# Performance work log

Measured on AMD Instinct MI355X. Metric: run time of the kernel, lower is better.

Reference implementation:

```python
import jax, jax.numpy as jnp
import numpy as np

N = 50000
E = 800000
IN_C = 1024
HID = 64
HEADS = 4
OUT_C = 64
NEG_SLOPE = 0.2  # PyG GATConv default


def setup_inputs() -> dict:
    key = jax.random.key(0)
    ks = jax.random.split(key, 12)
    x = jax.random.normal(ks[0], (N, IN_C), dtype=jnp.float32)
    edge_index = jax.random.randint(ks[1], (2, E), 0, N, dtype=jnp.int64)
    s1 = 1.0 / np.sqrt(IN_C)
    s2 = 1.0 / np.sqrt(HEADS * HID)
    return {
        "x": x,
        "edge_index": edge_index,
        "W1": jax.random.normal(ks[2], (HEADS * HID, IN_C), dtype=jnp.float32) * s1,
        "a_src1": jax.random.normal(ks[3], (HEADS, HID), dtype=jnp.float32) * s2,
        "a_dst1": jax.random.normal(ks[4], (HEADS, HID), dtype=jnp.float32) * s2,
        "b1": jnp.zeros((HEADS * HID,), dtype=jnp.float32),
        "W2": jax.random.normal(ks[5], (OUT_C, HEADS * HID), dtype=jnp.float32) * s2,
        "a_src2": jax.random.normal(ks[6], (1, OUT_C), dtype=jnp.float32) * 0.1,
        "a_dst2": jax.random.normal(ks[7], (1, OUT_C), dtype=jnp.float32) * 0.1,
        "b2": jnp.zeros((OUT_C,), dtype=jnp.float32),
    }


def gat_conv(x, src, dst, W, a_src, a_dst, b, heads, concat):
    # x: [N, F_in]; src/dst: [E'] (self-loops already appended)
    n = x.shape[0]
    h = (x @ W.T).reshape(n, heads, -1)                 # [N, H, C]
    alpha_s = (h * a_src).sum(-1)                       # [N, H]
    alpha_d = (h * a_dst).sum(-1)                       # [N, H]
    e = jax.nn.leaky_relu(alpha_s[src] + alpha_d[dst], NEG_SLOPE)  # [E', H]
    # segment softmax over edges grouped by destination
    m = jax.ops.segment_max(e, dst, num_segments=n)     # [N, H]
    ex = jnp.exp(e - m[dst])
    denom = jax.ops.segment_sum(ex, dst, num_segments=n)
    alpha = ex / denom[dst]                             # [E', H]
    out = jax.ops.segment_sum(alpha[:, :, None] * h[src], dst, num_segments=n)  # [N, H, C]
    out = out.reshape(n, -1) if concat else out.mean(axis=1)
    return out + b


def reference(x, edge_index, W1, a_src1, a_dst1, b1, W2, a_src2, a_dst2, b2):
    n = x.shape[0]
    loop = jnp.arange(n, dtype=edge_index.dtype)
    src = jnp.concatenate([edge_index[0], loop])  # PyG add_self_loops=True
    dst = jnp.concatenate([edge_index[1], loop])
    # eval mode: dropout is identity
    h = gat_conv(x, src, dst, W1, a_src1, a_dst1, b1, HEADS, concat=True)
    h = jax.nn.elu(h)
    out = gat_conv(h, src, dst, W2, a_src2, a_dst2, b2, 1, concat=False)
    return out
```

## Files before the change

### kernel.cpp

```cpp
#include <hip/hip_runtime.h>
#include <hip/hip_bf16.h>
#include <math.h>

constexpr int IN_C = 1024;
constexpr int HEADS = 4;
constexpr int F1 = 256;
constexpr int OUT_C = 64;
constexpr float NEG = 0.2f;

using bf16x8 = __attribute__((ext_vector_type(8))) short;
using f32x4 = __attribute__((ext_vector_type(4))) float;

__device__ __forceinline__ float leaky(float x) { return x > 0.f ? x : NEG * x; }

__device__ __forceinline__ unsigned short bf16bits(float v) {
  __hip_bfloat16 b = __float2bfloat16(v);
  return *reinterpret_cast<unsigned short*>(&b);
}
__device__ __forceinline__ float bf2f(unsigned short u) {
  union { unsigned u; float f; } c; c.u = (unsigned)u << 16; return c.f;
}

#define GLD_LDS16(g, l)                                                        \
  __builtin_amdgcn_global_load_lds(                                            \
      (const __attribute__((address_space(1))) void*)(g),                      \
      (__attribute__((address_space(3))) void*)(l), 16, 0, 0)

__global__ void cvt_bf16_kernel(const float* __restrict__ in,
                                unsigned short* __restrict__ out, int n) {
  int i = blockIdx.x * blockDim.x + threadIdx.x;
  if (i < n) out[i] = bf16bits(in[i]);
}

constexpr int LDTA = 72;

__global__ __launch_bounds__(256, 2) void gemm1_mfma(const float* __restrict__ X,
                                                     const unsigned short* __restrict__ Wb,
                                                     unsigned short* __restrict__ Hb,
                                                     const float* __restrict__ a_src,
                                                     const float* __restrict__ a_dst,
                                                     float* __restrict__ as_out,
                                                     float* __restrict__ ad_out, int M) {
  __shared__ unsigned short As[64 * LDTA];
  __shared__ unsigned short Bs[256 * 64];
  const int tid = threadIdx.x;
  const int wave = tid >> 6;
  const int lane = tid & 63;
  const int m15 = lane & 15;
  const int q = lane >> 4;
  const int bm = blockIdx.x * 64;

  f32x4 acc[4][4];
#pragma unroll
  for (int i = 0; i < 4; ++i)
#pragma unroll
    for (int j = 0; j < 4; ++j) acc[i][j] = (f32x4){0.f, 0.f, 0.f, 0.f};

  const int ar = tid >> 2;
  const int acg = (tid & 3) * 16;
  const int agr = (bm + ar < M) ? (bm + ar) : (M - 1);
  const float* aptr = X + (size_t)agr * IN_C + acg;

  for (int kt = 0; kt < IN_C; kt += 64) {
    float4 a0 = *(const float4*)(aptr + kt + 0);
    float4 a1 = *(const float4*)(aptr + kt + 4);
    float4 a2 = *(const float4*)(aptr + kt + 8);
    float4 a3 = *(const float4*)(aptr + kt + 12);
#pragma unroll
    for (int p = 0; p < 8; ++p) {
      int s = p * 256 + tid;
      int r = s >> 3;
      int cb = s & 7;
      const unsigned short* g = Wb + (size_t)r * IN_C + kt + ((cb ^ (r & 7)) << 3);
      GLD_LDS16(g, &Bs[(p * 256 + wave * 64) * 8]);
    }
    union { uint4 u4[2]; __hip_bfloat162 h[8]; } pk;
    pk.h[0] = __float22bfloat162_rn(make_float2(a0.x, a0.y));
    pk.h[1] = __float22bfloat162_rn(make_float2(a0.z, a0.w));
    pk.h[2] = __float22bfloat162_rn(make_float2(a1.x, a1.y));
    pk.h[3] = __float22bfloat162_rn(make_float2(a1.z, a1.w));
    pk.h[4] = __float22bfloat162_rn(make_float2(a2.x, a2.y));
    pk.h[5] = __float22bfloat162_rn(make_float2(a2.z, a2.w));
    pk.h[6] = __float22bfloat162_rn(make_float2(a3.x, a3.y));
    pk.h[7] = __float22bfloat162_rn(make_float2(a3.z, a3.w));
    *(uint4*)&As[ar * LDTA + acg] = pk.u4[0];
    *(uint4*)&As[ar * LDTA + acg + 8] = pk.u4[1];
    __syncthreads();

#pragma unroll
    for (int k0 = 0; k0 < 64; k0 += 32) {
      bf16x8 af[4], bfr[4];
#pragma unroll
      for (int i = 0; i < 4; ++i)
        af[i] = *(const bf16x8*)&As[(i * 16 + m15) * LDTA + k0 + q * 8];
#pragma unroll
      for (int j = 0; j < 4; ++j) {
        int rb = wave * 64 + j * 16 + m15;
        int cbp = ((k0 >> 3) + q) ^ (rb & 7);
        bfr[j] = *(const bf16x8*)&Bs[rb * 64 + cbp * 8];
      }
#pragma unroll
      for (int i = 0; i < 4; ++i)
#pragma unroll
        for (int j = 0; j < 4; ++j)
          acc[i][j] = __builtin_amdgcn_mfma_f32_16x16x32_bf16(af[i], bfr[j], acc[i][j], 0, 0, 0);
    }
    __syncthreads();
  }
  float asf[4], adf[4];
#pragma unroll
  for (int j = 0; j < 4; ++j) {
    asf[j] = a_src[wave * 64 + j * 16 + m15];
    adf[j] = a_dst[wave * 64 + j * 16 + m15];
  }
#pragma unroll
  for (int i = 0; i < 4; ++i) {
#pragma unroll
    for (int r = 0; r < 4; ++r) {
      int row = bm + i * 16 + q * 4 + r;
      if (row < M) {
#pragma unroll
        for (int j = 0; j < 4; ++j)
          Hb[(size_t)row * F1 + wave * 64 + j * 16 + m15] = bf16bits(acc[i][j][r]);
      }
      float s = acc[i][0][r] * asf[0] + acc[i][1][r] * asf[1] +
                acc[i][2][r] * asf[2] + acc[i][3][r] * asf[3];
      float d = acc[i][0][r] * adf[0] + acc[i][1][r] * adf[1] +
                acc[i][2][r] * adf[2] + acc[i][3][r] * adf[3];
#pragma unroll
      for (int o = 1; o < 16; o <<= 1) {
        s += __shfl_xor(s, o, 64);
        d += __shfl_xor(d, o, 64);
      }
      if (m15 == 0 && row < M) {
        as_out[row * HEADS + wave] = s;
        ad_out[row * HEADS + wave] = d;
      }
    }
  }
}

__global__ __launch_bounds__(256, 4) void gemm2_mfma(const unsigned short* __restrict__ Y,
                                                     const unsigned short* __restrict__ W2b,
                                                     float* __restrict__ H2,
                                                     const float* __restrict__ a_src,
                                                     const float* __restrict__ a_dst,
                                                     float* __restrict__ as_out,
                                                     float* __restrict__ ad_out, int M) {
  __shared__ unsigned short As[64 * 64];
  __shared__ unsigned short Bs[64 * 64];
  const int tid = threadIdx.x;
  const int wave = tid >> 6;
  const int lane = tid & 63;
  const int m15 = lane & 15;
  const int q = lane >> 4;
  const int bm = blockIdx.x * 64;

  f32x4 acc[4];
#pragma unroll
  for (int j = 0; j < 4; ++j) acc[j] = (f32x4){0.f, 0.f, 0.f, 0.f};

  for (int kt = 0; kt < F1; kt += 64) {
#pragma unroll
    for (int p = 0; p < 2; ++p) {
      int s = p * 256 + tid;
      int r = s >> 3;
      int cb = s & 7;
      int colo = (cb ^ (r & 7)) << 3;
      int gr = (bm + r < M) ? (bm + r) : (M - 1);
      GLD_LDS16(Y + (size_t)gr * F1 + kt + colo, &As[(p * 256 + wave * 64) * 8]);
      GLD_LDS16(W2b + (size_t)r * F1 + kt + colo, &Bs[(p * 256 + wave * 64) * 8]);
    }
    __syncthreads();
#pragma unroll
    for (int k0 = 0; k0 < 64; k0 += 32) {
      int ra = wave * 16 + m15;
      bf16x8 af = *(const bf16x8*)&As[ra * 64 + ((((k0 >> 3) + q) ^ (ra & 7)) << 3)];
      bf16x8 bfr[4];
#pragma unroll
      for (int j = 0; j < 4; ++j) {
        int rb = j * 16 + m15;
        bfr[j] = *(const bf16x8*)&Bs[rb * 64 + ((((k0 >> 3) + q) ^ (rb & 7)) << 3)];
      }
#pragma unroll
      for (int j = 0; j < 4; ++j)
        acc[j] = __builtin_amdgcn_mfma_f32_16x16x32_bf16(af, bfr[j], acc[j], 0, 0, 0);
    }
    __syncthreads();
  }
  float asf[4], adf[4];
#pragma unroll
  for (int j = 0; j < 4; ++j) {
    asf[j] = a_src[j * 16 + m15];
    adf[j] = a_dst[j * 16 + m15];
  }
#pragma unroll
  for (int r = 0; r < 4; ++r) {
    int row = bm + wave * 16 + q * 4 + r;
    if (row < M) {
#pragma unroll
      for (int j = 0; j < 4; ++j) H2[(size_t)row * OUT_C + j * 16 + m15] = acc[j][r];
    }
    float s = acc[0][r] * asf[0] + acc[1][r] * asf[1] + acc[2][r] * asf[2] + acc[3][r] * asf[3];
    float d = acc[0][r] * adf[0] + acc[1][r] * adf[1] + acc[2][r] * adf[2] + acc[3][r] * adf[3];
#pragma unroll
    for (int o = 1; o < 16; o <<= 1) {
      s += __shfl_xor(s, o, 64);
      d += __shfl_xor(d, o, 64);
    }
    if (m15 == 0 && row < M) {
      as_out[row] = s;
      ad_out[row] = d;
    }
  }
}

__global__ void degree_kernel(const int* __restrict__ ei, int E, int N,
                              int* __restrict__ deg) {
  int e = blockIdx.x * blockDim.x + threadIdx.x;
  if (e >= E + N) return;
  int dst = (e < E) ? ei[E + e] : (e - E);
  atomicAdd(&deg[dst], 1);
}

__global__ __launch_bounds__(256) void scan_block_sums(const int* __restrict__ deg,
                                                       int* __restrict__ part, int n) {
  __shared__ int sm[256];
  int t = threadIdx.x;
  int i = blockIdx.x * 256 + t;
  sm[t] = (i < n) ? deg[i] : 0;
  __syncthreads();
  for (int off = 128; off > 0; off >>= 1) {
    if (t < off) sm[t] += sm[t + off];
    __syncthreads();
  }
  if (t == 0) part[blockIdx.x] = sm[0];
}

__global__ __launch_bounds__(256) void scan_partials(int* __restrict__ part, int P) {
  __shared__ int sm[256];
  int t = threadIdx.x;
  int v = (t < P) ? part[t] : 0;
  sm[t] = v;
  __syncthreads();
  for (int off = 1; off < 256; off <<= 1) {
    int u = (t >= off) ? sm[t - off] : 0;
    __syncthreads();
    sm[t] += u;
    __syncthreads();
  }
  if (t < P) part[t] = sm[t];
}

__global__ __launch_bounds__(256) void scan_final(const int* __restrict__ deg,
                                                  const int* __restrict__ part,
                                                  int* __restrict__ row_ptr, int n) {
  __shared__ int sm[256];
  int t = threadIdx.x;
  int i = blockIdx.x * 256 + t;
  sm[t] = (i < n) ? deg[i] : 0;
  __syncthreads();
  for (int off = 1; off < 256; off <<= 1) {
    int u = (t >= off) ? sm[t - off] : 0;
    __syncthreads();
    sm[t] += u;
    __syncthreads();
  }
  int base = blockIdx.x ? part[blockIdx.x - 1] : 0;
  if (i < n) row_ptr[i + 1] = base + sm[t];
  if (i == 0) row_ptr[0] = 0;
}

__global__ void scatter_kernel(const int* __restrict__ ei, int E, int N,
                               const int* __restrict__ row_ptr, int* __restrict__ fill,
                               int* __restrict__ col) {
  int e = blockIdx.x * blockDim.x + threadIdx.x;
  if (e >= E + N) return;
  int src, dst;
  if (e < E) { src = ei[e]; dst = ei[E + e]; }
  else       { src = e - E; dst = e - E; }
  int pos = row_ptr[dst] + atomicAdd(&fill[dst], 1);
  col[pos] = src;
}

__global__ __launch_bounds__(256) void agg1_kernel(const unsigned short* __restrict__ hb,
                                                   const float* __restrict__ as,
                                                   const float* __restrict__ ad,
                                                   const int* __restrict__ row_ptr,
                                                   const int* __restrict__ col,
                                                   const float* __restrict__ bias,
                                                   unsigned short* __restrict__ yb, int N) {
  int dst = (blockIdx.x * blockDim.x + threadIdx.x) >> 6;
  int lane = threadIdx.x & 63;
  if (dst >= N) return;
  const int s0 = row_ptr[dst], s1 = row_ptr[dst + 1];
  const int par = lane >> 5;
  const int cg = lane & 31;
  const int hh = cg >> 3;
  const float adl = ad[dst * 4 + hh];
  float acc[8];
#pragma unroll
  for (int k = 0; k < 8; ++k) acc[k] = 0.f;
  float den = 0.f;

  int i = s0 + par;
  for (; i + 2 < s1; i += 4) {
    int sA = col[i], sB = col[i + 2];
    float wA = __expf(leaky(as[sA * 4 + hh] + adl));
    float wB = __expf(leaky(as[sB * 4 + hh] + adl));
    uint4 hA = *(const uint4*)(hb + (size_t)sA * F1 + cg * 8);
    uint4 hB = *(const uint4*)(hb + (size_t)sB * F1 + cg * 8);
    den += wA + wB;
    const unsigned short* pa = (const unsigned short*)&hA;
    const unsigned short* pb = (const unsigned short*)&hB;
#pragma unroll
    for (int k = 0; k < 8; ++k) {
      acc[k] = fmaf(wA, bf2f(pa[k]), acc[k]);
      acc[k] = fmaf(wB, bf2f(pb[k]), acc[k]);
    }
  }
  for (; i < s1; i += 2) {
    int s = col[i];
    float w = __expf(leaky(as[s * 4 + hh] + adl));
    uint4 hv = *(const uint4*)(hb + (size_t)s * F1 + cg * 8);
    den += w;
    const unsigned short* p = (const unsigned short*)&hv;
#pragma unroll
    for (int k = 0; k < 8; ++k) acc[k] = fmaf(w, bf2f(p[k]), acc[k]);
  }
  den += __shfl_xor(den, 32, 64);
#pragma unroll
  for (int k = 0; k < 8; ++k) acc[k] += __shfl_xor(acc[k], 32, 64);

  if (par == 0) {
    const float iv = 1.f / den;
    float4 b0 = *(const float4*)(bias + cg * 8);
    float4 b1 = *(const float4*)(bias + cg * 8 + 4);
    float bv[8] = {b0.x, b0.y, b0.z, b0.w, b1.x, b1.y, b1.z, b1.w};
    ushort4 o[2];
    unsigned short* po = (unsigned short*)o;
#pragma unroll
    for (int k = 0; k < 8; ++k) {
      float v = acc[k] * iv + bv[k];
      v = v > 0.f ? v : (__expf(v) - 1.f);
      po[k] = bf16bits(v);
    }
    *(uint4*)(yb + (size_t)dst * F1 + cg * 8) = *(uint4*)o;
  }
}

__global__ __launch_bounds__(256) void agg2_kernel(const float* __restrict__ h,
                                                   const float* __restrict__ as,
                                                   const float* __restrict__ ad,
                                                   const int* __restrict__ row_ptr,
                                                   const int* __restrict__ col,
                                                   const float* __restrict__ bias,
                                                   float* __restrict__ out, int N) {
  int dst = (blockIdx.x * blockDim.x + threadIdx.x) >> 6;
  int lane = threadIdx.x & 63;
  if (dst >= N) return;
  const int s0 = row_ptr[dst], s1 = row_ptr[dst + 1];
  const int par = lane >> 5;
  const int cg = lane & 31;
  const float adl = ad[dst];
  float a0 = 0.f, a1 = 0.f, den = 0.f;

  int i = s0 + par;
  for (; i + 2 < s1; i += 4) {
    int sA = col[i], sB = col[i + 2];
    float wA = __expf(leaky(as[sA] + adl));
    float wB = __expf(leaky(as[sB] + adl));
    float2 hA = *(const float2*)(h + (size_t)sA * OUT_C + cg * 2);
    float2 hB = *(const float2*)(h + (size_t)sB * OUT_C + cg * 2);
    den += wA + wB;
    a0 = fmaf(wA, hA.x, a0); a1 = fmaf(wA, hA.y, a1);
    a0 = fmaf(wB, hB.x, a0); a1 = fmaf(wB, hB.y, a1);
  }
  for (; i < s1; i += 2) {
    int s = col[i];
    float w = __expf(leaky(as[s] + adl));
    float2 hv = *(const float2*)(h + (size_t)s * OUT_C + cg * 2);
    den += w;
    a0 = fmaf(w, hv.x, a0); a1 = fmaf(w, hv.y, a1);
  }
  den += __shfl_xor(den, 32, 64);
  a0 += __shfl_xor(a0, 32, 64);
  a1 += __shfl_xor(a1, 32, 64);
  if (par == 0) {
    const float iv = 1.f / den;
    float2 bv = *(const float2*)(bias + cg * 2);
    float2 o = make_float2(a0 * iv + bv.x, a1 * iv + bv.y);
    *(float2*)(out + (size_t)dst * OUT_C + cg * 2) = o;
  }
}

extern "C" void kernel_launch(void* const* d_in, const int* in_sizes, int n_in,
                              void* d_out, int out_size, void* d_ws, size_t ws_size,
                              hipStream_t stream) {
  const float* x      = (const float*)d_in[0];
  const int*   ei     = (const int*)d_in[1];
  const float* W1     = (const float*)d_in[2];
  const float* a_src1 = (const float*)d_in[3];
  const float* a_dst1 = (const float*)d_in[4];
  const float* b1     = (const float*)d_in[5];
  const float* W2     = (const float*)d_in[6];
  const float* a_src2 = (const float*)d_in[7];
  const float* a_dst2 = (const float*)d_in[8];
  const float* b2     = (const float*)d_in[9];
  float* out = (float*)d_out;

  const int N = in_sizes[0] / IN_C;
  const int E = in_sizes[1] / 2;
  const int ET = E + N;

  char* ws = (char*)d_ws;
  size_t off = 0;
  auto alloc = [&](size_t bytes) -> void* {
    void* p = ws + off;
    off = (off + bytes + 255) & ~(size_t)255;
    return p;
  };
  unsigned short* h1b = (unsigned short*)alloc((size_t)N * F1 * 2);
  unsigned short* y1b = (unsigned short*)alloc((size_t)N * F1 * 2);
  float* h2      = (float*)alloc((size_t)N * OUT_C * 4);
  float* as1     = (float*)alloc((size_t)N * HEADS * 4);
  float* ad1     = (float*)alloc((size_t)N * HEADS * 4);
  float* as2     = (float*)alloc((size_t)N * 4);
  float* ad2     = (float*)alloc((size_t)N * 4);
  int*   deg     = (int*)alloc((size_t)N * 4);
  int*   row_ptr = (int*)alloc((size_t)(N + 1) * 4);
  int*   fill    = (int*)alloc((size_t)N * 4);
  int*   col     = (int*)alloc((size_t)ET * 4);
  int*   part    = (int*)alloc(1024 * 4);
  unsigned short* W1b = (unsigned short*)alloc((size_t)F1 * IN_C * 2);
  unsigned short* W2b = (unsigned short*)alloc((size_t)OUT_C * F1 * 2);
  (void)off; (void)ws_size; (void)n_in; (void)out_size;

  hipMemsetAsync(deg, 0, (size_t)N * 4, stream);
  hipMemsetAsync(fill, 0, (size_t)N * 4, stream);

  cvt_bf16_kernel<<<(F1 * IN_C + 255) / 256, 256, 0, stream>>>(W1, W1b, F1 * IN_C);
  cvt_bf16_kernel<<<(OUT_C * F1 + 255) / 256, 256, 0, stream>>>(W2, W2b, OUT_C * F1);

  const int P = (N + 255) / 256;
  degree_kernel<<<(ET + 255) / 256, 256, 0, stream>>>(ei, E, N, deg);
  scan_block_sums<<<P, 256, 0, stream>>>(deg, part, N);
  scan_partials<<<1, 256, 0, stream>>>(part, P);
  scan_final<<<P, 256, 0, stream>>>(deg, part, row_ptr, N);
  scatter_kernel<<<(ET + 255) / 256, 256, 0, stream>>>(ei, E, N, row_ptr, fill, col);

  const int NB4 = (N + 3) / 4;

  gemm1_mfma<<<(N + 63) / 64, 256, 0, stream>>>(x, W1b, h1b, a_src1, a_dst1, as1, ad1, N);
  agg1_kernel<<<NB4, 256, 0, stream>>>(h1b, as1, ad1, row_ptr, col, b1, y1b, N);

  gemm2_mfma<<<(N + 63) / 64, 256, 0, stream>>>(y1b, W2b, h2, a_src2, a_dst2, as2, ad2, N);
  agg2_kernel<<<NB4, 256, 0, stream>>>(h2, as2, ad2, row_ptr, col, b2, out, N);
}
```

Before: 540.6 us.

## Pre-shuffle weights into MFMA fragment layout and double-buffer A tiles

Weights are converted to bf16 in a fragment-ordered layout, so each lane can load its B operand straight from global memory (served from cache) instead of staging it through LDS. This frees the 32KB B buffer in gemm1, which allows the launch bound to rise from 2 to 3 blocks per SM and leaves room for a double-buffered A tile. The next X tile is now prefetched while the current one is multiplied, and gemm2 gets the same direct-from-global B loads. The risk is extra global/L2 traffic for B in every block, plus added register pressure under the tighter launch bound.

```diff
diff --git a/kernel.cpp b/kernel.cpp
--- a/kernel.cpp
+++ b/kernel.cpp
@@ -26,23 +26,34 @@
       (const __attribute__((address_space(1))) void*)(g),                      \
       (__attribute__((address_space(3))) void*)(l), 16, 0, 0)
 
-__global__ void cvt_bf16_kernel(const float* __restrict__ in,
-                                unsigned short* __restrict__ out, int n) {
-  int i = blockIdx.x * blockDim.x + threadIdx.x;
-  if (i < n) out[i] = bf16bits(in[i]);
+__global__ void shuf_w_kernel(const float* __restrict__ W,
+                              unsigned short* __restrict__ out, int K, int Nt) {
+  int idx = blockIdx.x * 256 + threadIdx.x;
+  int total = (K >> 5) * Nt * 64;
+  if (idx >= total) return;
+  int lane = idx & 63;
+  int rest = idx >> 6;
+  int n16 = rest % Nt;
+  int kc = rest / Nt;
+  int row = n16 * 16 + (lane & 15);
+  int colb = kc * 32 + (lane >> 4) * 8;
+  const float* src = W + (size_t)row * K + colb;
+  unsigned short tmp[8];
+#pragma unroll
+  for (int t = 0; t < 8; ++t) tmp[t] = bf16bits(src[t]);
+  *(uint4*)(out + (size_t)idx * 8) = *(uint4*)tmp;
 }
 
 constexpr int LDTA = 72;
 
-__global__ __launch_bounds__(256, 2) void gemm1_mfma(const float* __restrict__ X,
-                                                     const unsigned short* __restrict__ Wb,
+__global__ __launch_bounds__(256, 3) void gemm1_mfma(const float* __restrict__ X,
+                                                     const unsigned short* __restrict__ Wsh,
                                                      unsigned short* __restrict__ Hb,
                                                      const float* __restrict__ a_src,
                                                      const float* __restrict__ a_dst,
                                                      float* __restrict__ as_out,
                                                      float* __restrict__ ad_out, int M) {
-  __shared__ unsigned short As[64 * LDTA];
-  __shared__ unsigned short Bs[256 * 64];
+  __shared__ unsigned short As[2][64 * LDTA];
   const int tid = threadIdx.x;
   const int wave = tid >> 6;
   const int lane = tid & 63;
@@ -60,20 +71,13 @@
   const int acg = (tid & 3) * 16;
   const int agr = (bm + ar < M) ? (bm + ar) : (M - 1);
   const float* aptr = X + (size_t)agr * IN_C + acg;
-
-  for (int kt = 0; kt < IN_C; kt += 64) {
-    float4 a0 = *(const float4*)(aptr + kt + 0);
-    float4 a1 = *(const float4*)(aptr + kt + 4);
-    float4 a2 = *(const float4*)(aptr + kt + 8);
-    float4 a3 = *(const float4*)(aptr + kt + 12);
-#pragma unroll
-    for (int p = 0; p < 8; ++p) {
-      int s = p * 256 + tid;
-      int r = s >> 3;
-      int cb = s & 7;
-      const unsigned short* g = Wb + (size_t)r * IN_C + kt + ((cb ^ (r & 7)) << 3);
-      GLD_LDS16(g, &Bs[(p * 256 + wave * 64) * 8]);
-    }
+  const unsigned short* bbase = Wsh + ((size_t)(wave * 4) * 64 + lane) * 8;
+
+  {
+    float4 a0 = *(const float4*)(aptr + 0);
+    float4 a1 = *(const float4*)(aptr + 4);
+    float4 a2 = *(const float4*)(aptr + 8);
+    float4 a3 = *(const float4*)(aptr + 12);
     union { uint4 u4[2]; __hip_bfloat162 h[8]; } pk;
     pk.h[0] = __float22bfloat162_rn(make_float2(a0.x, a0.y));
     pk.h[1] = __float22bfloat162_rn(make_float2(a0.z, a0.w));
@@ -83,30 +87,55 @@
     pk.h[5] = __float22bfloat162_rn(make_float2(a2.z, a2.w));
     pk.h[6] = __float22bfloat162_rn(make_float2(a3.x, a3.y));
     pk.h[7] = __float22bfloat162_rn(make_float2(a3.z, a3.w));
-    *(uint4*)&As[ar * LDTA + acg] = pk.u4[0];
-    *(uint4*)&As[ar * LDTA + acg + 8] = pk.u4[1];
-    __syncthreads();
-
+    *(uint4*)&As[0][ar * LDTA + acg] = pk.u4[0];
+    *(uint4*)&As[0][ar * LDTA + acg + 8] = pk.u4[1];
+  }
+  __syncthreads();
+
+  int p = 0;
+  for (int kt = 0; kt < IN_C; kt += 64) {
+    const bool more = (kt + 64) < IN_C;
+    float4 a0, a1, a2, a3;
+    if (more) {
+      a0 = *(const float4*)(aptr + kt + 64);
+      a1 = *(const float4*)(aptr + kt + 68);
+      a2 = *(const float4*)(aptr + kt + 72);
+      a3 = *(const float4*)(aptr + kt + 76);
+    }
+    const int kc0 = kt >> 5;
 #pragma unroll
     for (int k0 = 0; k0 < 64; k0 += 32) {
+      const int kc = kc0 + (k0 >> 5);
       bf16x8 af[4], bfr[4];
 #pragma unroll
+      for (int j = 0; j < 4; ++j)
+        bfr[j] = *(const bf16x8*)(bbase + (size_t)kc * 8192 + j * 512);
+#pragma unroll
       for (int i = 0; i < 4; ++i)
-        af[i] = *(const bf16x8*)&As[(i * 16 + m15) * LDTA + k0 + q * 8];
-#pragma unroll
-      for (int j = 0; j < 4; ++j) {
-        int rb = wave * 64 + j * 16 + m15;
-        int cbp = ((k0 >> 3) + q) ^ (rb & 7);
-        bfr[j] = *(const bf16x8*)&Bs[rb * 64 + cbp * 8];
-      }
+        af[i] = *(const bf16x8*)&As[p][(i * 16 + m15) * LDTA + k0 + q * 8];
 #pragma unroll
       for (int i = 0; i < 4; ++i)
 #pragma unroll
         for (int j = 0; j < 4; ++j)
           acc[i][j] = __builtin_amdgcn_mfma_f32_16x16x32_bf16(af[i], bfr[j], acc[i][j], 0, 0, 0);
     }
-    __syncthreads();
-  }
+    if (more) {
+      union { uint4 u4[2]; __hip_bfloat162 h[8]; } pk;
+      pk.h[0] = __float22bfloat162_rn(make_float2(a0.x, a0.y));
+      pk.h[1] = __float22bfloat162_rn(make_float2(a0.z, a0.w));
+      pk.h[2] = __float22bfloat162_rn(make_float2(a1.x, a1.y));
+      pk.h[3] = __float22bfloat162_rn(make_float2(a1.z, a1.w));
+      pk.h[4] = __float22bfloat162_rn(make_float2(a2.x, a2.y));
+      pk.h[5] = __float22bfloat162_rn(make_float2(a2.z, a2.w));
+      pk.h[6] = __float22bfloat162_rn(make_float2(a3.x, a3.y));
+      pk.h[7] = __float22bfloat162_rn(make_float2(a3.z, a3.w));
+      *(uint4*)&As[p ^ 1][ar * LDTA + acg] = pk.u4[0];
+      *(uint4*)&As[p ^ 1][ar * LDTA + acg + 8] = pk.u4[1];
+    }
+    __syncthreads();
+    p ^= 1;
+  }
+
   float asf[4], adf[4];
 #pragma unroll
   for (int j = 0; j < 4; ++j) {
@@ -141,14 +170,13 @@
 }
 
 __global__ __launch_bounds__(256, 4) void gemm2_mfma(const unsigned short* __restrict__ Y,
-                                                     const unsigned short* __restrict__ W2b,
+                                                     const unsigned short* __restrict__ W2sh,
                                                      float* __restrict__ H2,
                                                      const float* __restrict__ a_src,
                                                      const float* __restrict__ a_dst,
                                                      float* __restrict__ as_out,
                                                      float* __restrict__ ad_out, int M) {
   __shared__ unsigned short As[64 * 64];
-  __shared__ unsigned short Bs[64 * 64];
   const int tid = threadIdx.x;
   const int wave = tid >> 6;
   const int lane = tid & 63;
@@ -159,6 +187,7 @@
   f32x4 acc[4];
 #pragma unroll
   for (int j = 0; j < 4; ++j) acc[j] = (f32x4){0.f, 0.f, 0.f, 0.f};
+  const unsigned short* bbase = W2sh + ((size_t)lane) * 8;
 
   for (int kt = 0; kt < F1; kt += 64) {
 #pragma unroll
@@ -169,19 +198,17 @@
       int colo = (cb ^ (r & 7)) << 3;
       int gr = (bm + r < M) ? (bm + r) : (M - 1);
       GLD_LDS16(Y + (size_t)gr * F1 + kt + colo, &As[(p * 256 + wave * 64) * 8]);
-      GLD_LDS16(W2b + (size_t)r * F1 + kt + colo, &Bs[(p * 256 + wave * 64) * 8]);
     }
     __syncthreads();
 #pragma unroll
     for (int k0 = 0; k0 < 64; k0 += 32) {
+      const int kc = (kt + k0) >> 5;
       int ra = wave * 16 + m15;
       bf16x8 af = *(const bf16x8*)&As[ra * 64 + ((((k0 >> 3) + q) ^ (ra & 7)) << 3)];
       bf16x8 bfr[4];
 #pragma unroll
-      for (int j = 0; j < 4; ++j) {
-        int rb = j * 16 + m15;
-        bfr[j] = *(const bf16x8*)&Bs[rb * 64 + ((((k0 >> 3) + q) ^ (rb & 7)) << 3)];
-      }
+      for (int j = 0; j < 4; ++j)
+        bfr[j] = *(const bf16x8*)(bbase + (size_t)kc * 2048 + j * 512);
 #pragma unroll
       for (int j = 0; j < 4; ++j)
         acc[j] = __builtin_amdgcn_mfma_f32_16x16x32_bf16(af, bfr[j], acc[j], 0, 0, 0);
@@ -432,15 +459,15 @@
   int*   fill    = (int*)alloc((size_t)N * 4);
   int*   col     = (int*)alloc((size_t)ET * 4);
   int*   part    = (int*)alloc(1024 * 4);
-  unsigned short* W1b = (unsigned short*)alloc((size_t)F1 * IN_C * 2);
-  unsigned short* W2b = (unsigned short*)alloc((size_t)OUT_C * F1 * 2);
+  unsigned short* W1sh = (unsigned short*)alloc((size_t)F1 * IN_C * 2);
+  unsigned short* W2sh = (unsigned short*)alloc((size_t)OUT_C * F1 * 2);
   (void)off; (void)ws_size; (void)n_in; (void)out_size;
 
   hipMemsetAsync(deg, 0, (size_t)N * 4, stream);
   hipMemsetAsync(fill, 0, (size_t)N * 4, stream);
 
-  cvt_bf16_kernel<<<(F1 * IN_C + 255) / 256, 256, 0, stream>>>(W1, W1b, F1 * IN_C);
-  cvt_bf16_kernel<<<(OUT_C * F1 + 255) / 256, 256, 0, stream>>>(W2, W2b, OUT_C * F1);
+  shuf_w_kernel<<<(32 * 16 * 64 + 255) / 256, 256, 0, stream>>>(W1, W1sh, IN_C, 16);
+  shuf_w_kernel<<<(8 * 4 * 64 + 255) / 256, 256, 0, stream>>>(W2, W2sh, F1, 4);
 
   const int P = (N + 255) / 256;
   degree_kernel<<<(ET + 255) / 256, 256, 0, stream>>>(ei, E, N, deg);
@@ -451,9 +478,9 @@
 
   const int NB4 = (N + 3) / 4;
 
-  gemm1_mfma<<<(N + 63) / 64, 256, 0, stream>>>(x, W1b, h1b, a_src1, a_dst1, as1, ad1, N);
+  gemm1_mfma<<<(N + 63) / 64, 256, 0, stream>>>(x, W1sh, h1b, a_src1, a_dst1, as1, ad1, N);
   agg1_kernel<<<NB4, 256, 0, stream>>>(h1b, as1, ad1, row_ptr, col, b1, y1b, N);
 
-  gemm2_mfma<<<(N + 63) / 64, 256, 0, stream>>>(y1b, W2b, h2, a_src2, a_dst2, as2, ad2, N);
+  gemm2_mfma<<<(N + 63) / 64, 256, 0, stream>>>(y1b, W2sh, h2, a_src2, a_dst2, as2, ad2, N);
   agg2_kernel<<<NB4, 256, 0, stream>>>(h2, as2, ad2, row_ptr, col, b2, out, N);
 }
```

Measured after the change: 542.3 us. About the same (+0.3%).
